# Kernel optimization log

Measured on AMD Instinct MI355X. Metric: run time of the kernel, lower is better.

Reference implementation:

```python
import jax, jax.numpy as jnp
import numpy as np

B, T, L, D = 4, 8, 512, 512
H, KD, VD = 8, 64, 64


def setup_inputs() -> dict:
    key = jax.random.key(0)
    ks = jax.random.split(key, 8)
    s = 0.05
    return {
        "queries": jax.random.normal(ks[0], (B, T, L, D), jnp.float32),
        "keys": jax.random.normal(ks[1], (B, T, L, D), jnp.float32),
        "values": jax.random.normal(ks[2], (B, T, L, D), jnp.float32),
        "attn_mask": jnp.ones((1, 1, 1, L, L), jnp.float32),
        "Wq": jax.random.normal(ks[3], (D, H, KD), jnp.float32) * s,
        "Wk": jax.random.normal(ks[4], (D, H, KD), jnp.float32) * s,
        "Wv": jax.random.normal(ks[5], (D, H, VD), jnp.float32) * s,
        "w_head": jax.random.normal(ks[6], (H,), jnp.float32),
        "tau": jnp.ones((1,), jnp.float32),
        "delta": jnp.zeros((1,), jnp.float32),
    }


def reference(queries, keys, values, attn_mask, Wq, Wk, Wv, w_head, tau, delta):
    # Projections: (b,t,l,d) x (d,h,e) -> (b,t,l,h,e)
    Q = jnp.einsum('btld,dhe->btlhe', queries, Wq)
    K = jnp.einsum('btld,dhe->btlhe', keys, Wk)
    V = jnp.einsum('btld,dhe->btlhe', values, Wv)
    scale = 1.0 / jnp.sqrt(jnp.asarray(KD, jnp.float32))
    # Full score tensor (b,t,h,l,s)
    scores = jnp.einsum('btlhe,btshe->bthls', Q, K)
    # de-stationary rescaling, then scale, then multiplicative mask
    scores = (scores * tau[0] + delta[0]) * scale
    scores = scores * attn_mask
    # Dropout(attn_dropout) before softmax is identity at inference
    p = jax.nn.softmax(scores, axis=-1)
    attn = jnp.einsum('bthls,btshe->bthle', p, V)
    # Per-head scalar weighted sum over heads: (b,t,h,l,e),(h)->(b,t,l,e)
    return jnp.einsum('bthle,h->btle', attn, w_head)
```

## Files before the change

kernel.cpp:

```cpp
#include <hip/hip_runtime.h>
#include <hip/hip_bf16.h>

typedef __bf16 bf16;
typedef __bf16 bf16x4 __attribute__((ext_vector_type(4)));
typedef __bf16 bf16x8 __attribute__((ext_vector_type(8)));
typedef float f32x4 __attribute__((ext_vector_type(4)));


#if __has_builtin(__builtin_amdgcn_exp2f)
#define EXP2(x) __builtin_amdgcn_exp2f(x)
#else
#define EXP2(x) exp2f(x)
#endif

static __device__ __forceinline__ f32x4 mfma16(bf16x4 a, bf16x4 b, f32x4 c) {
#if __has_builtin(__builtin_amdgcn_mfma_f32_16x16x16bf16_1k)
    return __builtin_amdgcn_mfma_f32_16x16x16bf16_1k(a, b, c, 0, 0, 0);
#else
    asm("v_mfma_f32_16x16x16_bf16 %0, %1, %2, %0" : "+v"(c) : "v"(a), "v"(b));
    return c;
#endif
}

__global__ __launch_bounds__(256) void prep_kernel(const float* __restrict__ W0,
                                                   const float* __restrict__ W1,
                                                   const float* __restrict__ W2,
                                                   const float* __restrict__ maskf,
                                                   bf16* __restrict__ Wt,
                                                   bf16* __restrict__ Mp) {
    if (blockIdx.z == 3) {
        const int bid = blockIdx.y * 8 + blockIdx.x;
        const int t0 = bid * 256 + threadIdx.x;
        const float4* m4 = (const float4*)maskf;
#pragma unroll
        for (int j = 0; j < 4; ++j) {
            int idx = t0 + j * 16384;
            int q = idx >> 7;
            int sc = idx & 127;
            int cc = sc >> 4;
            int ns = (sc >> 2) & 3;
            int qd = sc & 3;
            float4 v = m4[idx];
            bf16x4 o;
            o[0] = (bf16)v.x; o[1] = (bf16)v.y; o[2] = (bf16)v.z; o[3] = (bf16)v.w;
            size_t off = ((((size_t)(q >> 4) * 8 + cc) * 4 + ns) * 4 + qd) * 64 +
                         (q & 15) * 4;
            *(bf16x4*)&Mp[off] = o;
        }
        return;
    }
    __shared__ float t[64][65];
    const float* W = (blockIdx.z == 0) ? W0 : (blockIdx.z == 1) ? W1 : W2;
    bf16* O = Wt + (size_t)blockIdx.z * 512 * 512;
    const int d0 = blockIdx.x * 64, n0 = blockIdx.y * 64;
    {
        int nl = threadIdx.x & 63, dg = threadIdx.x >> 6;
#pragma unroll
        for (int j = 0; j < 16; ++j) {
            int dl = dg + j * 4;
            t[nl][dl] = W[(size_t)(d0 + dl) * 512 + n0 + nl];
        }
    }
    __syncthreads();
    {
        int dl = threadIdx.x & 63, ng = threadIdx.x >> 6;
#pragma unroll
        for (int j = 0; j < 16; ++j) {
            int nl = ng + j * 4;
            O[(size_t)(n0 + nl) * 512 + d0 + dl] = (bf16)t[nl][dl];
        }
    }
}

__global__ __launch_bounds__(256) void proj_kernel(
    const float* __restrict__ Xq, const float* __restrict__ Xk,
    const float* __restrict__ Xv, const bf16* __restrict__ Wt,
    bf16* __restrict__ Qw, bf16* __restrict__ Kw, bf16* __restrict__ Vt) {
    __shared__ __align__(16) bf16 smem[18432];
    bf16* la = smem;
    bf16* lb = smem + 128 * 72;

    const float* X = (blockIdx.z == 0) ? Xq : (blockIdx.z == 1) ? Xk : Xv;
    const bf16* W  = Wt + (size_t)blockIdx.z * 512 * 512;
    bf16* Out      = (blockIdx.z == 0) ? Qw : (blockIdx.z == 1) ? Kw : Vt;

    const int tid = threadIdx.x, wave = tid >> 6, lane = tid & 63;
    const int quad = lane >> 4, lc = lane & 15;
    const int wm = wave & 1, wn = wave >> 1;
    const int bid = blockIdx.x + (blockIdx.y << 7);
    const int jj = bid >> 3;
    const int yy = jj & 3;
    const int xt = (bid & 7) * 16 + (jj >> 2);
    const int m0 = xt * 128, n0 = yy * 128;

    f32x4 acc[4][4];
#pragma unroll
    for (int ms = 0; ms < 4; ++ms)
#pragma unroll
        for (int ns = 0; ns < 4; ++ns) acc[ms][ns] = (f32x4){0.f, 0.f, 0.f, 0.f};

    const int ar = tid >> 4, ac = tid & 15;
    const int br = tid >> 3, bc = tid & 7;

    float4 xr[8];
    bf16x8 wr[4];
#pragma unroll
    for (int i = 0; i < 8; ++i)
        xr[i] = *(const float4*)&X[(size_t)(m0 + ar + i * 16) * 512 + ac * 4];
#pragma unroll
    for (int i = 0; i < 4; ++i)
        wr[i] = *(const bf16x8*)&W[(size_t)(n0 + br + i * 32) * 512 + bc * 8];

    for (int kb = 0; kb < 512; kb += 64) {
        __syncthreads();
#pragma unroll
        for (int i = 0; i < 8; ++i) {
            float4 x = xr[i];
            bf16x4 p;
            p[0] = (bf16)x.x; p[1] = (bf16)x.y; p[2] = (bf16)x.z; p[3] = (bf16)x.w;
            *(bf16x4*)&la[(ar + i * 16) * 72 + ac * 4] = p;
        }
#pragma unroll
        for (int i = 0; i < 4; ++i)
            *(bf16x8*)&lb[(br + i * 32) * 72 + bc * 8] = wr[i];
        __syncthreads();
        if (kb < 448) {
            int kn = kb + 64;
#pragma unroll
            for (int i = 0; i < 8; ++i)
                xr[i] = *(const float4*)&X[(size_t)(m0 + ar + i * 16) * 512 + kn + ac * 4];
#pragma unroll
            for (int i = 0; i < 4; ++i)
                wr[i] = *(const bf16x8*)&W[(size_t)(n0 + br + i * 32) * 512 + kn + bc * 8];
        }
#pragma unroll
        for (int kk = 0; kk < 2; ++kk) {
            bf16x8 af[4], bfr[4];
#pragma unroll
            for (int ms = 0; ms < 4; ++ms)
                af[ms] = *(bf16x8*)&la[(wm * 64 + ms * 16 + lc) * 72 + kk * 32 + quad * 8];
#pragma unroll
            for (int ns = 0; ns < 4; ++ns)
                bfr[ns] = *(bf16x8*)&lb[(wn * 64 + ns * 16 + lc) * 72 + kk * 32 + quad * 8];
#pragma unroll
            for (int ms = 0; ms < 4; ++ms)
#pragma unroll
                for (int ns = 0; ns < 4; ++ns)
                    acc[ms][ns] = __builtin_amdgcn_mfma_f32_16x16x32_bf16(
                        af[ms], bfr[ns], acc[ms][ns], 0, 0, 0);
        }
    }
    __syncthreads();
    bf16* lds_c = smem;
    if (blockIdx.z != 2) {
#pragma unroll
        for (int ms = 0; ms < 4; ++ms)
#pragma unroll
            for (int ns = 0; ns < 4; ++ns)
#pragma unroll
                for (int r = 0; r < 4; ++r)
                    lds_c[(wm * 64 + ms * 16 + quad * 4 + r) * 136 +
                          wn * 64 + ns * 16 + lc] = (bf16)acc[ms][ns][r];
    } else {
#pragma unroll
        for (int ms = 0; ms < 4; ++ms)
#pragma unroll
            for (int ns = 0; ns < 4; ++ns)
#pragma unroll
                for (int r = 0; r < 4; ++r)
                    lds_c[(wn * 64 + ns * 16 + lc) * 136 +
                          wm * 64 + ms * 16 + quad * 4 + r] = (bf16)acc[ms][ns][r];
    }
    __syncthreads();
    const int bt = m0 >> 9, l0 = m0 & 511;
    if (blockIdx.z != 2) {
        const int ec = tid & 7, rg = tid >> 3;
#pragma unroll
        for (int hc = 0; hc < 2; ++hc) {
            int h = (n0 >> 6) + hc;
#pragma unroll
            for (int p = 0; p < 4; ++p) {
                int row = rg + p * 32;
                bf16x8 v = *(bf16x8*)&lds_c[row * 136 + hc * 64 + ec * 8];
                *(bf16x8*)&Out[(((size_t)bt * 8 + h) * 512 + l0 + row) * 64 + ec * 8] = v;
            }
        }
    } else {
        const int rowp = lane >> 2, cc = lane & 3;
#pragma unroll
        for (int pr = 0; pr < 2; ++pr) {
            int row = wave * 32 + pr * 16 + rowp;
            int h = (n0 >> 6) + (row >> 6);
            int e = row & 63;
            bf16* dst = Out + (((size_t)bt * 8 + h) * 64 + e) * 512 + l0;
#pragma unroll
            for (int pc = 0; pc < 4; ++pc) {
                int mc = cc + pc * 4;
                *(bf16x8*)&dst[mc * 8] = *(bf16x8*)&lds_c[row * 136 + mc * 8];
            }
        }
    }
}

__global__ __launch_bounds__(256, 4) void attn_kernel(
    const bf16* __restrict__ Qw, const bf16* __restrict__ Kw,
    const bf16* __restrict__ Vt, const bf16* __restrict__ Mp,
    const float* __restrict__ w_head, const float* __restrict__ tau,
    const float* __restrict__ delta, float* __restrict__ out) {
    __shared__ __align__(16) bf16 lds_k[2][64 * 72];
    __shared__ __align__(16) bf16 lds_vt[2][64 * 72];

    const int tid  = threadIdx.x;
    const int wave = tid >> 6;
    const int lane = tid & 63;
    const int quad = lane >> 4;
    const int lc   = lane & 15;
    const int b    = blockIdx.x;
    const int bth  = b & 255;
    const int qquad = b >> 8;
    const int bt   = bth >> 3;
    const int h    = bth & 7;

    const bf16* Qh  = Qw + (size_t)bth * (512 * 64);
    const bf16* Kh  = Kw + (size_t)bth * (512 * 64);
    const bf16* VtH = Vt + (size_t)bth * (512 * 64);

    const float L2E = 1.4426950408889634f;
    const float ts = tau[0] * 0.125f * L2E;
    const float ds = delta[0] * 0.125f * L2E;
    const float wh = w_head[h];

    const int q0 = qquad * 128 + wave * 32;
    const size_t mbA = (size_t)(q0 >> 4) * 8192 + lane * 4;
    const size_t mbB = mbA + 8192;

    bf16x8 qfA[2], qfB[2];
#pragma unroll
    for (int kk = 0; kk < 2; ++kk) {
        qfA[kk] = *(const bf16x8*)&Qh[(size_t)(q0 + lc) * 64 + kk * 32 + quad * 8];
        qfB[kk] = *(const bf16x8*)&Qh[(size_t)(q0 + 16 + lc) * 64 + kk * 32 + quad * 8];
    }

    f32x4 oA[4], oB[4];
#pragma unroll
    for (int ns = 0; ns < 4; ++ns) {
        oA[ns] = (f32x4){0.f, 0.f, 0.f, 0.f};
        oB[ns] = (f32x4){0.f, 0.f, 0.f, 0.f};
    }
    float lA = 0.f, lB = 0.f;

    const int srow = tid >> 3, scc = tid & 7;
    bf16x8 kr[2], vr[2];
    kr[0] = *(const bf16x8*)&Kh[(size_t)srow * 64 + scc * 8];
    kr[1] = *(const bf16x8*)&Kh[(size_t)(srow + 32) * 64 + scc * 8];
    vr[0] = *(const bf16x8*)&VtH[(size_t)srow * 512 + scc * 8];
    vr[1] = *(const bf16x8*)&VtH[(size_t)(srow + 32) * 512 + scc * 8];
    *(bf16x8*)&lds_k[0][srow * 72 + scc * 8] = kr[0];
    *(bf16x8*)&lds_k[0][(srow + 32) * 72 + scc * 8] = kr[1];
    *(bf16x8*)&lds_vt[0][srow * 72 + scc * 8] = vr[0];
    *(bf16x8*)&lds_vt[0][(srow + 32) * 72 + scc * 8] = vr[1];
    kr[0] = *(const bf16x8*)&Kh[(size_t)(64 + srow) * 64 + scc * 8];
    kr[1] = *(const bf16x8*)&Kh[(size_t)(64 + srow + 32) * 64 + scc * 8];
    vr[0] = *(const bf16x8*)&VtH[(size_t)srow * 512 + 64 + scc * 8];
    vr[1] = *(const bf16x8*)&VtH[(size_t)(srow + 32) * 512 + 64 + scc * 8];

    for (int c = 0; c < 8; ++c) {
        const int buf = c & 1;
        __syncthreads();
        bf16x4 mA[4], mB[4];
        {
            const size_t mc = mbA + (size_t)c * 1024;
            const size_t md = mbB + (size_t)c * 1024;
#pragma unroll
            for (int ns = 0; ns < 4; ++ns) {
                mA[ns] = *(const bf16x4*)&Mp[mc + ns * 256];
                mB[ns] = *(const bf16x4*)&Mp[md + ns * 256];
            }
        }
        f32x4 stA[4], stB[4];
#pragma unroll
        for (int ns = 0; ns < 4; ++ns) {
            stA[ns] = (f32x4){0.f, 0.f, 0.f, 0.f};
            stB[ns] = (f32x4){0.f, 0.f, 0.f, 0.f};
        }
#pragma unroll
        for (int kk = 0; kk < 2; ++kk)
#pragma unroll
            for (int ns = 0; ns < 4; ++ns) {
                bf16x8 ka = *(bf16x8*)&lds_k[buf][(ns * 16 + lc) * 72 + kk * 32 + quad * 8];
                stA[ns] = __builtin_amdgcn_mfma_f32_16x16x32_bf16(ka, qfA[kk], stA[ns], 0, 0, 0);
                stB[ns] = __builtin_amdgcn_mfma_f32_16x16x32_bf16(ka, qfB[kk], stB[ns], 0, 0, 0);
            }
        if (c < 7) {
            const int nb = buf ^ 1;
            *(bf16x8*)&lds_k[nb][srow * 72 + scc * 8] = kr[0];
            *(bf16x8*)&lds_k[nb][(srow + 32) * 72 + scc * 8] = kr[1];
            *(bf16x8*)&lds_vt[nb][srow * 72 + scc * 8] = vr[0];
            *(bf16x8*)&lds_vt[nb][(srow + 32) * 72 + scc * 8] = vr[1];
            if (c < 6) {
                const int s0n = (c + 2) * 64;
                kr[0] = *(const bf16x8*)&Kh[(size_t)(s0n + srow) * 64 + scc * 8];
                kr[1] = *(const bf16x8*)&Kh[(size_t)(s0n + srow + 32) * 64 + scc * 8];
                vr[0] = *(const bf16x8*)&VtH[(size_t)srow * 512 + s0n + scc * 8];
                vr[1] = *(const bf16x8*)&VtH[(size_t)(srow + 32) * 512 + s0n + scc * 8];
            }
        }
        bf16x4 paA[4], paB[4];
#pragma unroll
        for (int ns = 0; ns < 4; ++ns) {
#pragma unroll
            for (int r = 0; r < 4; ++r) {
                float eA = (stA[ns][r] * ts + ds) * (float)mA[ns][r];
                float eB = (stB[ns][r] * ts + ds) * (float)mB[ns][r];
                float pA = EXP2(eA);
                float pB = EXP2(eB);
                lA += pA; lB += pB;
                paA[ns][r] = (bf16)pA;
                paB[ns][r] = (bf16)pB;
            }
        }
#pragma unroll
        for (int ks = 0; ks < 4; ++ks)
#pragma unroll
            for (int ns = 0; ns < 4; ++ns) {
                bf16x4 vv = *(bf16x4*)&lds_vt[buf][(ns * 16 + lc) * 72 + ks * 16 + quad * 4];
                oA[ns] = mfma16(paA[ks], vv, oA[ns]);
                oB[ns] = mfma16(paB[ks], vv, oB[ns]);
            }
    }
    lA += __shfl_xor(lA, 16, 64);
    lA += __shfl_xor(lA, 32, 64);
    lB += __shfl_xor(lB, 16, 64);
    lB += __shfl_xor(lB, 32, 64);
#pragma unroll
    for (int r = 0; r < 4; ++r) {
        float lrA = __shfl(lA, quad * 4 + r, 64);
        float lrB = __shfl(lB, quad * 4 + r, 64);
        float ivA = wh / lrA, ivB = wh / lrB;
        int qqA = q0 + quad * 4 + r;
        int qqB = q0 + 16 + quad * 4 + r;
#pragma unroll
        for (int ns = 0; ns < 4; ++ns) {
            int e = ns * 16 + lc;
            atomicAdd(&out[((size_t)bt * 512 + qqA) * 64 + e], oA[ns][r] * ivA);
            atomicAdd(&out[((size_t)bt * 512 + qqB) * 64 + e], oB[ns][r] * ivB);
        }
    }
}

extern "C" void kernel_launch(void* const* d_in, const int* in_sizes, int n_in,
                              void* d_out, int out_size, void* d_ws, size_t ws_size,
                              hipStream_t stream) {
    const float* queries = (const float*)d_in[0];
    const float* keys    = (const float*)d_in[1];
    const float* values  = (const float*)d_in[2];
    const float* mask    = (const float*)d_in[3];
    const float* Wq      = (const float*)d_in[4];
    const float* Wk      = (const float*)d_in[5];
    const float* Wv      = (const float*)d_in[6];
    const float* w_head  = (const float*)d_in[7];
    const float* tau     = (const float*)d_in[8];
    const float* delta   = (const float*)d_in[9];

    char* ws = (char*)d_ws;
    bf16* Qw = (bf16*)(ws);
    bf16* Kw = (bf16*)(ws + 16777216ull);
    bf16* Vt = (bf16*)(ws + 33554432ull);
    bf16* Wt = (bf16*)(ws + 50331648ull);
    bf16* Mp = (bf16*)(ws + 51904512ull);

    hipMemsetAsync(d_out, 0, (size_t)out_size * sizeof(float), stream);

    prep_kernel<<<dim3(8, 8, 4), 256, 0, stream>>>(Wq, Wk, Wv, mask, Wt, Mp);

    proj_kernel<<<dim3(128, 4, 3), 256, 0, stream>>>(queries, keys, values, Wt,
                                                     Qw, Kw, Vt);

    attn_kernel<<<1024, 256, 0, stream>>>(Qw, Kw, Vt, Mp, w_head, tau, delta,
                                          (float*)d_out);
}
```

Before: 229.8 us.

## Replace head-sum atomics with per-head partial buffer and reduction kernel

Instead of each attention block atomically adding its weighted head output into the final tensor, blocks write per-head partials (fp32 or fp16 depending on workspace size) to a scratch buffer, and a separate reduce kernel sums the 8 heads. This removes atomic contention and the memset, at the cost of extra global traffic for the partial buffer and an additional kernel launch. The fp16 path adds rounding error to the partials.

```diff
diff --git a/kernel.cpp b/kernel.cpp
--- a/kernel.cpp
+++ b/kernel.cpp
@@ -5,6 +5,7 @@
 typedef __bf16 bf16x4 __attribute__((ext_vector_type(4)));
 typedef __bf16 bf16x8 __attribute__((ext_vector_type(8)));
 typedef float f32x4 __attribute__((ext_vector_type(4)));
+typedef _Float16 half4 __attribute__((ext_vector_type(4)));
 
 
 #if __has_builtin(__builtin_amdgcn_exp2f)
@@ -206,7 +207,8 @@
     const bf16* __restrict__ Qw, const bf16* __restrict__ Kw,
     const bf16* __restrict__ Vt, const bf16* __restrict__ Mp,
     const float* __restrict__ w_head, const float* __restrict__ tau,
-    const float* __restrict__ delta, float* __restrict__ out) {
+    const float* __restrict__ delta, float* __restrict__ out,
+    void* __restrict__ opart, int mode) {
     __shared__ __align__(16) bf16 lds_k[2][64 * 72];
     __shared__ __align__(16) bf16 lds_vt[2][64 * 72];
 
@@ -339,13 +341,54 @@
         float ivA = wh / lrA, ivB = wh / lrB;
         int qqA = q0 + quad * 4 + r;
         int qqB = q0 + 16 + quad * 4 + r;
-#pragma unroll
-        for (int ns = 0; ns < 4; ++ns) {
-            int e = ns * 16 + lc;
-            atomicAdd(&out[((size_t)bt * 512 + qqA) * 64 + e], oA[ns][r] * ivA);
-            atomicAdd(&out[((size_t)bt * 512 + qqB) * 64 + e], oB[ns][r] * ivB);
-        }
-    }
+        if (mode == 0) {
+#pragma unroll
+            for (int ns = 0; ns < 4; ++ns) {
+                int e = ns * 16 + lc;
+                atomicAdd(&out[((size_t)bt * 512 + qqA) * 64 + e], oA[ns][r] * ivA);
+                atomicAdd(&out[((size_t)bt * 512 + qqB) * 64 + e], oB[ns][r] * ivB);
+            }
+        } else if (mode == 1) {
+            float* op = (float*)opart;
+#pragma unroll
+            for (int ns = 0; ns < 4; ++ns) {
+                int e = ns * 16 + lc;
+                op[((size_t)bth * 512 + qqA) * 64 + e] = oA[ns][r] * ivA;
+                op[((size_t)bth * 512 + qqB) * 64 + e] = oB[ns][r] * ivB;
+            }
+        } else {
+            _Float16* op = (_Float16*)opart;
+#pragma unroll
+            for (int ns = 0; ns < 4; ++ns) {
+                int e = ns * 16 + lc;
+                op[((size_t)bth * 512 + qqA) * 64 + e] = (_Float16)(oA[ns][r] * ivA);
+                op[((size_t)bth * 512 + qqB) * 64 + e] = (_Float16)(oB[ns][r] * ivB);
+            }
+        }
+    }
+}
+
+__global__ __launch_bounds__(256) void reduce_kernel(const void* __restrict__ part,
+                                                     float* __restrict__ out,
+                                                     int mode) {
+    const int idx = blockIdx.x * 256 + threadIdx.x;
+    const int bt = idx >> 13;
+    const int rf = idx & 8191;
+    f32x4 s = (f32x4){0.f, 0.f, 0.f, 0.f};
+    if (mode == 1) {
+        const f32x4* p = (const f32x4*)part + (size_t)bt * 65536 + rf;
+#pragma unroll
+        for (int h = 0; h < 8; ++h) s += p[(size_t)h * 8192];
+    } else {
+        const half4* p = (const half4*)part + (size_t)bt * 65536 + rf;
+#pragma unroll
+        for (int h = 0; h < 8; ++h) {
+            half4 v = p[(size_t)h * 8192];
+            s[0] += (float)v[0]; s[1] += (float)v[1];
+            s[2] += (float)v[2]; s[3] += (float)v[3];
+        }
+    }
+    *(f32x4*)&out[(size_t)idx * 4] = s;
 }
 
 extern "C" void kernel_launch(void* const* d_in, const int* in_sizes, int n_in,
@@ -368,8 +411,13 @@
     bf16* Vt = (bf16*)(ws + 33554432ull);
     bf16* Wt = (bf16*)(ws + 50331648ull);
     bf16* Mp = (bf16*)(ws + 51904512ull);
-
-    hipMemsetAsync(d_out, 0, (size_t)out_size * sizeof(float), stream);
+    char* Op = ws + 52428800ull;
+
+    int mode = (ws_size >= 52428800ull + 33554432ull) ? 1
+             : (ws_size >= 52428800ull + 16777216ull) ? 2 : 0;
+
+    if (mode == 0)
+        hipMemsetAsync(d_out, 0, (size_t)out_size * sizeof(float), stream);
 
     prep_kernel<<<dim3(8, 8, 4), 256, 0, stream>>>(Wq, Wk, Wv, mask, Wt, Mp);
 
@@ -377,5 +425,9 @@
                                                      Qw, Kw, Vt);
 
     attn_kernel<<<1024, 256, 0, stream>>>(Qw, Kw, Vt, Mp, w_head, tau, delta,
-                                          (float*)d_out);
-}
+                                          (float*)d_out, (void*)Op, mode);
+
+    if (mode != 0)
+        reduce_kernel<<<1024, 256, 0, stream>>>((const void*)Op, (float*)d_out,
+                                                mode);
+}
```

Result: faster. 224.6 us (-2.2%).

## Fuse prep, projection, attention into cooperative persistent kernel with head-reduction pass

Applied to the files above, without the earlier changes.

Merges the three kernels plus the output memset into one cooperative mega-kernel that uses grid-wide syncs between the weight/mask prep, projection, attention, and reduction phases. It also replaces per-head fp32 atomicAdds into the output with fp16 per-head partial stores followed by a separate reduction over heads. The aim is to remove launch gaps, the memset, and atomic contention. In exchange it adds grid.sync costs, loses overlap between stages, stores partials in fp16 (lower precision), and may cap occupancy for the projection and attention phases.

```diff
diff --git a/kernel.cpp b/kernel.cpp
--- a/kernel.cpp
+++ b/kernel.cpp
@@ -1,10 +1,14 @@
 #include <hip/hip_runtime.h>
 #include <hip/hip_bf16.h>
+#include <hip/hip_cooperative_groups.h>
+
+namespace cg = cooperative_groups;
 
 typedef __bf16 bf16;
 typedef __bf16 bf16x4 __attribute__((ext_vector_type(4)));
 typedef __bf16 bf16x8 __attribute__((ext_vector_type(8)));
 typedef float f32x4 __attribute__((ext_vector_type(4)));
+typedef _Float16 half4 __attribute__((ext_vector_type(4)));
 
 
 #if __has_builtin(__builtin_amdgcn_exp2f)
@@ -22,37 +26,16 @@
 #endif
 }
 
-__global__ __launch_bounds__(256) void prep_kernel(const float* __restrict__ W0,
-                                                   const float* __restrict__ W1,
-                                                   const float* __restrict__ W2,
-                                                   const float* __restrict__ maskf,
-                                                   bf16* __restrict__ Wt,
-                                                   bf16* __restrict__ Mp) {
-    if (blockIdx.z == 3) {
-        const int bid = blockIdx.y * 8 + blockIdx.x;
-        const int t0 = bid * 256 + threadIdx.x;
-        const float4* m4 = (const float4*)maskf;
-#pragma unroll
-        for (int j = 0; j < 4; ++j) {
-            int idx = t0 + j * 16384;
-            int q = idx >> 7;
-            int sc = idx & 127;
-            int cc = sc >> 4;
-            int ns = (sc >> 2) & 3;
-            int qd = sc & 3;
-            float4 v = m4[idx];
-            bf16x4 o;
-            o[0] = (bf16)v.x; o[1] = (bf16)v.y; o[2] = (bf16)v.z; o[3] = (bf16)v.w;
-            size_t off = ((((size_t)(q >> 4) * 8 + cc) * 4 + ns) * 4 + qd) * 64 +
-                         (q & 15) * 4;
-            *(bf16x4*)&Mp[off] = o;
-        }
-        return;
-    }
-    __shared__ float t[64][65];
-    const float* W = (blockIdx.z == 0) ? W0 : (blockIdx.z == 1) ? W1 : W2;
-    bf16* O = Wt + (size_t)blockIdx.z * 512 * 512;
-    const int d0 = blockIdx.x * 64, n0 = blockIdx.y * 64;
+
+static __device__ __forceinline__ void prep_w_job(int job, const float* W0,
+                                                  const float* W1, const float* W2,
+                                                  bf16* Wt, char* sraw) {
+    float(*t)[65] = (float(*)[65])sraw;
+    __syncthreads();
+    const int z = job >> 6, sub = job & 63;
+    const float* W = (z == 0) ? W0 : (z == 1) ? W1 : W2;
+    bf16* O = Wt + (size_t)z * 512 * 512;
+    const int d0 = (sub & 7) * 64, n0 = (sub >> 3) * 64;
     {
         int nl = threadIdx.x & 63, dg = threadIdx.x >> 6;
 #pragma unroll
@@ -72,22 +55,46 @@
     }
 }
 
-__global__ __launch_bounds__(256) void proj_kernel(
-    const float* __restrict__ Xq, const float* __restrict__ Xk,
-    const float* __restrict__ Xv, const bf16* __restrict__ Wt,
-    bf16* __restrict__ Qw, bf16* __restrict__ Kw, bf16* __restrict__ Vt) {
-    __shared__ __align__(16) bf16 smem[18432];
+static __device__ __forceinline__ void prep_mask_job(int bid, const float* maskf,
+                                                     bf16* Mp) {
+    const int t0 = bid * 256 + threadIdx.x;
+    const float4* m4 = (const float4*)maskf;
+#pragma unroll
+    for (int j = 0; j < 4; ++j) {
+        int idx = t0 + j * 16384;
+        int q = idx >> 7;
+        int sc = idx & 127;
+        int cc = sc >> 4;
+        int ns = (sc >> 2) & 3;
+        int qd = sc & 3;
+        float4 v = m4[idx];
+        bf16x4 o;
+        o[0] = (bf16)v.x; o[1] = (bf16)v.y; o[2] = (bf16)v.z; o[3] = (bf16)v.w;
+        size_t off = ((((size_t)(q >> 4) * 8 + cc) * 4 + ns) * 4 + qd) * 64 +
+                     (q & 15) * 4;
+        *(bf16x4*)&Mp[off] = o;
+    }
+}
+
+static __device__ __forceinline__ void proj_job(int j, const float* __restrict__ Xq,
+                                                const float* __restrict__ Xk,
+                                                const float* __restrict__ Xv,
+                                                const bf16* __restrict__ Wt,
+                                                bf16* __restrict__ Qw,
+                                                bf16* __restrict__ Kw,
+                                                bf16* __restrict__ Vt, char* sraw) {
+    bf16* smem = (bf16*)sraw;
     bf16* la = smem;
-    bf16* lb = smem + 128 * 72;
-
-    const float* X = (blockIdx.z == 0) ? Xq : (blockIdx.z == 1) ? Xk : Xv;
-    const bf16* W  = Wt + (size_t)blockIdx.z * 512 * 512;
-    bf16* Out      = (blockIdx.z == 0) ? Qw : (blockIdx.z == 1) ? Kw : Vt;
+    bf16* lb = smem + 9216;
+
+    const int z = j >> 9, bid = j & 511;
+    const float* X = (z == 0) ? Xq : (z == 1) ? Xk : Xv;
+    const bf16* W  = Wt + (size_t)z * 512 * 512;
+    bf16* Out      = (z == 0) ? Qw : (z == 1) ? Kw : Vt;
 
     const int tid = threadIdx.x, wave = tid >> 6, lane = tid & 63;
     const int quad = lane >> 4, lc = lane & 15;
     const int wm = wave & 1, wn = wave >> 1;
-    const int bid = blockIdx.x + (blockIdx.y << 7);
     const int jj = bid >> 3;
     const int yy = jj & 3;
     const int xt = (bid & 7) * 16 + (jj >> 2);
@@ -152,7 +159,7 @@
     }
     __syncthreads();
     bf16* lds_c = smem;
-    if (blockIdx.z != 2) {
+    if (z != 2) {
 #pragma unroll
         for (int ms = 0; ms < 4; ++ms)
 #pragma unroll
@@ -173,7 +180,7 @@
     }
     __syncthreads();
     const int bt = m0 >> 9, l0 = m0 & 511;
-    if (blockIdx.z != 2) {
+    if (z != 2) {
         const int ec = tid & 7, rg = tid >> 3;
 #pragma unroll
         for (int hc = 0; hc < 2; ++hc) {
@@ -202,20 +209,21 @@
     }
 }
 
-__global__ __launch_bounds__(256, 4) void attn_kernel(
-    const bf16* __restrict__ Qw, const bf16* __restrict__ Kw,
+static __device__ __forceinline__ void attn_job(
+    int b, const bf16* __restrict__ Qw, const bf16* __restrict__ Kw,
     const bf16* __restrict__ Vt, const bf16* __restrict__ Mp,
     const float* __restrict__ w_head, const float* __restrict__ tau,
-    const float* __restrict__ delta, float* __restrict__ out) {
-    __shared__ __align__(16) bf16 lds_k[2][64 * 72];
-    __shared__ __align__(16) bf16 lds_vt[2][64 * 72];
+    const float* __restrict__ delta, float* __restrict__ out,
+    _Float16* __restrict__ Op, int mode, char* sraw) {
+    bf16* ldsK = (bf16*)sraw;
+    bf16* ldsV = (bf16*)sraw + 9216;
+    __syncthreads();
 
     const int tid  = threadIdx.x;
     const int wave = tid >> 6;
     const int lane = tid & 63;
     const int quad = lane >> 4;
     const int lc   = lane & 15;
-    const int b    = blockIdx.x;
     const int bth  = b & 255;
     const int qquad = b >> 8;
     const int bt   = bth >> 3;
@@ -255,10 +263,10 @@
     kr[1] = *(const bf16x8*)&Kh[(size_t)(srow + 32) * 64 + scc * 8];
     vr[0] = *(const bf16x8*)&VtH[(size_t)srow * 512 + scc * 8];
     vr[1] = *(const bf16x8*)&VtH[(size_t)(srow + 32) * 512 + scc * 8];
-    *(bf16x8*)&lds_k[0][srow * 72 + scc * 8] = kr[0];
-    *(bf16x8*)&lds_k[0][(srow + 32) * 72 + scc * 8] = kr[1];
-    *(bf16x8*)&lds_vt[0][srow * 72 + scc * 8] = vr[0];
-    *(bf16x8*)&lds_vt[0][(srow + 32) * 72 + scc * 8] = vr[1];
+    *(bf16x8*)&ldsK[srow * 72 + scc * 8] = kr[0];
+    *(bf16x8*)&ldsK[(srow + 32) * 72 + scc * 8] = kr[1];
+    *(bf16x8*)&ldsV[srow * 72 + scc * 8] = vr[0];
+    *(bf16x8*)&ldsV[(srow + 32) * 72 + scc * 8] = vr[1];
     kr[0] = *(const bf16x8*)&Kh[(size_t)(64 + srow) * 64 + scc * 8];
     kr[1] = *(const bf16x8*)&Kh[(size_t)(64 + srow + 32) * 64 + scc * 8];
     vr[0] = *(const bf16x8*)&VtH[(size_t)srow * 512 + 64 + scc * 8];
@@ -266,6 +274,8 @@
 
     for (int c = 0; c < 8; ++c) {
         const int buf = c & 1;
+        bf16* lk = ldsK + buf * 4608;
+        bf16* lv = ldsV + buf * 4608;
         __syncthreads();
         bf16x4 mA[4], mB[4];
         {
@@ -287,16 +297,17 @@
         for (int kk = 0; kk < 2; ++kk)
 #pragma unroll
             for (int ns = 0; ns < 4; ++ns) {
-                bf16x8 ka = *(bf16x8*)&lds_k[buf][(ns * 16 + lc) * 72 + kk * 32 + quad * 8];
+                bf16x8 ka = *(bf16x8*)&lk[(ns * 16 + lc) * 72 + kk * 32 + quad * 8];
                 stA[ns] = __builtin_amdgcn_mfma_f32_16x16x32_bf16(ka, qfA[kk], stA[ns], 0, 0, 0);
                 stB[ns] = __builtin_amdgcn_mfma_f32_16x16x32_bf16(ka, qfB[kk], stB[ns], 0, 0, 0);
             }
         if (c < 7) {
-            const int nb = buf ^ 1;
-            *(bf16x8*)&lds_k[nb][srow * 72 + scc * 8] = kr[0];
-            *(bf16x8*)&lds_k[nb][(srow + 32) * 72 + scc * 8] = kr[1];
-            *(bf16x8*)&lds_vt[nb][srow * 72 + scc * 8] = vr[0];
-            *(bf16x8*)&lds_vt[nb][(srow + 32) * 72 + scc * 8] = vr[1];
+            bf16* lkn = ldsK + (buf ^ 1) * 4608;
+            bf16* lvn = ldsV + (buf ^ 1) * 4608;
+            *(bf16x8*)&lkn[srow * 72 + scc * 8] = kr[0];
+            *(bf16x8*)&lkn[(srow + 32) * 72 + scc * 8] = kr[1];
+            *(bf16x8*)&lvn[srow * 72 + scc * 8] = vr[0];
+            *(bf16x8*)&lvn[(srow + 32) * 72 + scc * 8] = vr[1];
             if (c < 6) {
                 const int s0n = (c + 2) * 64;
                 kr[0] = *(const bf16x8*)&Kh[(size_t)(s0n + srow) * 64 + scc * 8];
@@ -323,7 +334,7 @@
         for (int ks = 0; ks < 4; ++ks)
 #pragma unroll
             for (int ns = 0; ns < 4; ++ns) {
-                bf16x4 vv = *(bf16x4*)&lds_vt[buf][(ns * 16 + lc) * 72 + ks * 16 + quad * 4];
+                bf16x4 vv = *(bf16x4*)&lv[(ns * 16 + lc) * 72 + ks * 16 + quad * 4];
                 oA[ns] = mfma16(paA[ks], vv, oA[ns]);
                 oB[ns] = mfma16(paB[ks], vv, oB[ns]);
             }
@@ -339,13 +350,96 @@
         float ivA = wh / lrA, ivB = wh / lrB;
         int qqA = q0 + quad * 4 + r;
         int qqB = q0 + 16 + quad * 4 + r;
-#pragma unroll
-        for (int ns = 0; ns < 4; ++ns) {
-            int e = ns * 16 + lc;
-            atomicAdd(&out[((size_t)bt * 512 + qqA) * 64 + e], oA[ns][r] * ivA);
-            atomicAdd(&out[((size_t)bt * 512 + qqB) * 64 + e], oB[ns][r] * ivB);
-        }
-    }
+        if (mode == 0) {
+#pragma unroll
+            for (int ns = 0; ns < 4; ++ns) {
+                int e = ns * 16 + lc;
+                atomicAdd(&out[((size_t)bt * 512 + qqA) * 64 + e], oA[ns][r] * ivA);
+                atomicAdd(&out[((size_t)bt * 512 + qqB) * 64 + e], oB[ns][r] * ivB);
+            }
+        } else {
+#pragma unroll
+            for (int ns = 0; ns < 4; ++ns) {
+                int e = ns * 16 + lc;
+                Op[((size_t)bth * 512 + qqA) * 64 + e] = (_Float16)(oA[ns][r] * ivA);
+                Op[((size_t)bth * 512 + qqB) * 64 + e] = (_Float16)(oB[ns][r] * ivB);
+            }
+        }
+    }
+}
+
+static __device__ __forceinline__ void reduce_one(int idx, const _Float16* __restrict__ Op,
+                                                  float* __restrict__ out) {
+    const int bt = idx >> 13, rf = idx & 8191;
+    const half4* p = (const half4*)Op + (size_t)bt * 65536 + rf;
+    f32x4 s = (f32x4){0.f, 0.f, 0.f, 0.f};
+#pragma unroll
+    for (int h = 0; h < 8; ++h) {
+        half4 v = p[(size_t)h * 8192];
+        s[0] += (float)v[0]; s[1] += (float)v[1];
+        s[2] += (float)v[2]; s[3] += (float)v[3];
+    }
+    *(f32x4*)&out[(size_t)idx * 4] = s;
+}
+
+__global__ __launch_bounds__(256, 4) void mega_kernel(
+    const float* __restrict__ Xq, const float* __restrict__ Xk,
+    const float* __restrict__ Xv, const float* __restrict__ maskf,
+    const float* __restrict__ Wq, const float* __restrict__ Wk,
+    const float* __restrict__ Wv, const float* __restrict__ w_head,
+    const float* __restrict__ tau, const float* __restrict__ delta,
+    float* __restrict__ out, bf16* __restrict__ Qw, bf16* __restrict__ Kw,
+    bf16* __restrict__ Vt, bf16* __restrict__ Wt, bf16* __restrict__ Mp,
+    _Float16* __restrict__ Op) {
+    __shared__ __align__(16) char sraw[36864];
+    cg::grid_group grid = cg::this_grid();
+    const int G = (int)gridDim.x;
+
+    for (int j = (int)blockIdx.x; j < 256; j += G) {
+        if (j < 192) prep_w_job(j, Wq, Wk, Wv, Wt, sraw);
+        else         prep_mask_job(j - 192, maskf, Mp);
+    }
+    grid.sync();
+    for (int j = (int)blockIdx.x; j < 1536; j += G)
+        proj_job(j, Xq, Xk, Xv, Wt, Qw, Kw, Vt, sraw);
+    grid.sync();
+    for (int j = (int)blockIdx.x; j < 1024; j += G)
+        attn_job(j, Qw, Kw, Vt, Mp, w_head, tau, delta, out, Op, 2, sraw);
+    grid.sync();
+    for (int i = (int)blockIdx.x * 256 + (int)threadIdx.x; i < 262144; i += G * 256)
+        reduce_one(i, Op, out);
+}
+
+__global__ __launch_bounds__(256) void prep_kernel(const float* W0, const float* W1,
+                                                   const float* W2, const float* maskf,
+                                                   bf16* Wt, bf16* Mp) {
+    __shared__ __align__(16) char sraw[36864];
+    if (blockIdx.z == 3) {
+        prep_mask_job(blockIdx.y * 8 + blockIdx.x, maskf, Mp);
+        return;
+    }
+    prep_w_job(blockIdx.z * 64 + blockIdx.y * 8 + blockIdx.x, W0, W1, W2, Wt, sraw);
+}
+
+__global__ __launch_bounds__(256) void proj_kernel(const float* Xq, const float* Xk,
+                                                   const float* Xv, const bf16* Wt,
+                                                   bf16* Qw, bf16* Kw, bf16* Vt) {
+    __shared__ __align__(16) char sraw[36864];
+    int j = blockIdx.z * 512 + blockIdx.y * 128 + blockIdx.x;
+    proj_job(j, Xq, Xk, Xv, Wt, Qw, Kw, Vt, sraw);
+}
+
+__global__ __launch_bounds__(256, 4) void attn_kernel(const bf16* Qw, const bf16* Kw,
+                                                      const bf16* Vt, const bf16* Mp,
+                                                      const float* w_head, const float* tau,
+                                                      const float* delta, float* out,
+                                                      _Float16* Op, int mode) {
+    __shared__ __align__(16) char sraw[36864];
+    attn_job(blockIdx.x, Qw, Kw, Vt, Mp, w_head, tau, delta, out, Op, mode, sraw);
+}
+
+__global__ __launch_bounds__(256) void reduce_kernel(const _Float16* Op, float* out) {
+    reduce_one(blockIdx.x * 256 + threadIdx.x, Op, out);
 }
 
 extern "C" void kernel_launch(void* const* d_in, const int* in_sizes, int n_in,
@@ -368,14 +462,50 @@
     bf16* Vt = (bf16*)(ws + 33554432ull);
     bf16* Wt = (bf16*)(ws + 50331648ull);
     bf16* Mp = (bf16*)(ws + 51904512ull);
-
-    hipMemsetAsync(d_out, 0, (size_t)out_size * sizeof(float), stream);
-
+    _Float16* Op = (_Float16*)(ws + 52428800ull);
+    float* outp = (float*)d_out;
+    const size_t need_mega = 52428800ull + 16777216ull;
+
+    static int s_grid = -2;
+    if (s_grid == -2) {
+        int dev = 0, coop = 0, cus = 0, mb = 0;
+        (void)hipGetDevice(&dev);
+        (void)hipDeviceGetAttribute(&coop, hipDeviceAttributeCooperativeLaunch, dev);
+        (void)hipDeviceGetAttribute(&cus, hipDeviceAttributeMultiprocessorCount, dev);
+        if (coop && cus > 0 &&
+            hipOccupancyMaxActiveBlocksPerMultiprocessor(&mb, mega_kernel, 256, 0) ==
+                hipSuccess &&
+            mb > 0) {
+            long g = (long)mb * (long)cus;
+            if (g > 1024) g = 1024;
+            s_grid = (int)g;
+        } else {
+            s_grid = 0;
+        }
+    }
+
+    if (ws_size >= need_mega && s_grid >= 256) {
+        void* params[] = {(void*)&queries, (void*)&keys,   (void*)&values,
+                          (void*)&mask,    (void*)&Wq,     (void*)&Wk,
+                          (void*)&Wv,      (void*)&w_head, (void*)&tau,
+                          (void*)&delta,   (void*)&outp,   (void*)&Qw,
+                          (void*)&Kw,      (void*)&Vt,     (void*)&Wt,
+                          (void*)&Mp,      (void*)&Op};
+        hipError_t e = hipLaunchCooperativeKernel(mega_kernel, dim3(s_grid),
+                                                  dim3(256), params, 0, stream);
+        if (e == hipSuccess) return;
+        (void)hipGetLastError();
+        s_grid = 0;
+    }
+
+    int mode = (ws_size >= need_mega) ? 2 : 0;
+    if (mode == 0)
+        hipMemsetAsync(d_out, 0, (size_t)out_size * sizeof(float), stream);
     prep_kernel<<<dim3(8, 8, 4), 256, 0, stream>>>(Wq, Wk, Wv, mask, Wt, Mp);
-
     proj_kernel<<<dim3(128, 4, 3), 256, 0, stream>>>(queries, keys, values, Wt,
                                                      Qw, Kw, Vt);
-
     attn_kernel<<<1024, 256, 0, stream>>>(Qw, Kw, Vt, Mp, w_head, tau, delta,
-                                          (float*)d_out);
-}
+                                          (float*)d_out, Op, mode);
+    if (mode != 0)
+        reduce_kernel<<<1024, 256, 0, stream>>>(Op, (float*)d_out);
+}
```

After: 513.9 us. +123.7%, slower.
